# Kernel optimization log

Hardware: AMD Instinct MI355X
Metric: run time of the kernel (lower is better)

The kernel has to match this reference:

```python
import jax, jax.numpy as jnp
import numpy as np

WS = 7      # window size
SHIFT = 3   # shift size
H = 56
W = 56
NH = 16     # num heads


def _layernorm(x, g, b):
    m = x.mean(-1, keepdims=True)
    v = x.var(-1, keepdims=True)
    return (x - m) / jnp.sqrt(v + 1e-5) * g + b


def setup_inputs() -> dict:
    key = jax.random.key(0)
    ks = jax.random.split(key, 8)
    B, C = 16, 512
    DH = 4 * C
    s = 0.02
    x = jax.random.normal(ks[0], (B, H * W, C), jnp.float32)

    # relative position index (matches torch buffer construction)
    coords = np.stack(np.meshgrid(np.arange(WS), np.arange(WS), indexing='ij')).reshape(2, -1)
    rel = (coords[:, :, None] - coords[:, None, :]).transpose(1, 2, 0).copy()
    rel[..., 0] += WS - 1
    rel[..., 1] += WS - 1
    rel[..., 0] *= 2 * WS - 1
    rpi = jnp.asarray(rel.sum(-1), jnp.int32)  # (49, 49)

    # shifted-window additive attention mask (nW, N, N)
    img = np.zeros((H, W))
    cnt = 0
    for hs in (slice(0, -WS), slice(-WS, -SHIFT), slice(-SHIFT, None)):
        for wsl in (slice(0, -WS), slice(-WS, -SHIFT), slice(-SHIFT, None)):
            img[hs, wsl] = cnt
            cnt += 1
    mw = img.reshape(H // WS, WS, W // WS, WS).transpose(0, 2, 1, 3).reshape(-1, WS * WS)
    diff = mw[:, None, :] - mw[:, :, None]  # == mw.unsqueeze(1) - mw.unsqueeze(2)
    attn_mask = jnp.asarray(np.where(diff != 0, -100.0, 0.0), jnp.float32)

    return {
        'x': x,
        'rpi': rpi,
        'attn_mask': attn_mask,
        'norm1_g': jnp.ones((C,), jnp.float32),
        'norm1_b': jnp.zeros((C,), jnp.float32),
        'qkv_w': jax.random.normal(ks[1], (3 * C, C), jnp.float32) * s,
        'qkv_b': jnp.zeros((3 * C,), jnp.float32),
        'proj_w': jax.random.normal(ks[2], (C, C), jnp.float32) * s,
        'proj_b': jnp.zeros((C,), jnp.float32),
        'rpb_table': jax.random.normal(ks[3], ((2 * WS - 1) ** 2, NH), jnp.float32) * s,
        'norm2_g': jnp.ones((C,), jnp.float32),
        'norm2_b': jnp.zeros((C,), jnp.float32),
        'mlp_w1': jax.random.normal(ks[4], (DH, C), jnp.float32) * s,
        'mlp_b1': jnp.zeros((DH,), jnp.float32),
        'mlp_w2': jax.random.normal(ks[5], (C, DH), jnp.float32) * s,
        'mlp_b2': jnp.zeros((C,), jnp.float32),
    }


def reference(x, rpi, attn_mask, norm1_g, norm1_b, qkv_w, qkv_b, proj_w, proj_b,
              rpb_table, norm2_g, norm2_b, mlp_w1, mlp_b1, mlp_w2, mlp_b2):
    B, L, C = x.shape
    N = WS * WS
    nW = (H // WS) * (W // WS)
    hd = C // NH

    # --- attention branch ---
    h = _layernorm(x, norm1_g, norm1_b).reshape(B, H, W, C)
    h = jnp.roll(h, (-SHIFT, -SHIFT), axis=(1, 2))
    # window partition -> (B*nW, N, C)
    xw = h.reshape(B, H // WS, WS, W // WS, WS, C).transpose(0, 1, 3, 2, 4, 5).reshape(B * nW, N, C)

    qkv = (xw @ qkv_w.T + qkv_b).reshape(B * nW, N, 3, NH, hd).transpose(2, 0, 3, 1, 4)
    q, k, v = qkv[0], qkv[1], qkv[2]  # (B*nW, NH, N, hd)
    attn = jnp.einsum('bhnd,bhmd->bhnm', q * (hd ** -0.5), k)
    rpb = rpb_table[rpi].transpose(2, 0, 1)  # (NH, N, N)
    attn = attn + rpb[None]
    attn = attn.reshape(B, nW, NH, N, N) + attn_mask[None, :, None]
    attn = jax.nn.softmax(attn.reshape(B * nW, NH, N, N), axis=-1)
    o = jnp.einsum('bhnm,bhmd->bhnd', attn, v).transpose(0, 2, 1, 3).reshape(B * nW, N, C)
    o = o @ proj_w.T + proj_b
    # window reverse + unshift
    o = o.reshape(B, H // WS, W // WS, WS, WS, C).transpose(0, 1, 3, 2, 4, 5).reshape(B, H, W, C)
    o = jnp.roll(o, (SHIFT, SHIFT), axis=(1, 2)).reshape(B, L, C)

    x = x + o
    # --- MLP branch ---
    h2 = _layernorm(x, norm2_g, norm2_b)
    m = jax.nn.gelu(h2 @ mlp_w1.T + mlp_b1, approximate=False)
    return x + (m @ mlp_w2.T + mlp_b2)
```

## Files before the change

kernel.cpp:

```cpp
#include <hip/hip_runtime.h>
#include <hip/hip_bf16.h>

typedef __attribute__((ext_vector_type(8))) short bf16x8_t;
typedef __attribute__((ext_vector_type(4))) float f32x4_t;

__device__ __forceinline__ void gll16(const void* g, void* l) {
  __builtin_amdgcn_global_load_lds((const __attribute__((address_space(1))) void*)g,
                                   (__attribute__((address_space(3))) void*)l, 16, 0, 0);
}

__global__ __launch_bounds__(256) void k_cvt(const float* __restrict__ in,
                                             __hip_bfloat16* __restrict__ out, int n) {
  int i = blockIdx.x * 256 + threadIdx.x;
  if (i < n) out[i] = __float2bfloat16(in[i]);
}

__global__ __launch_bounds__(256) void k_cmb(const int* __restrict__ rpi,
                                             const float* __restrict__ tab,
                                             const float* __restrict__ mask,
                                             float* __restrict__ cmbp) {
  int idx = blockIdx.x * 256 + threadIdx.x;
  int jj = idx & 3, lane = (idx >> 2) & 63, tile = (idx >> 8) & 15;
  int h = (idx >> 12) & 15, w6 = idx >> 16;
  int r = (tile >> 2) * 16 + (lane >> 4) * 4 + jj;
  int c = (tile & 3) * 16 + (lane & 15);
  float v = -1e9f;
  if (r < 49 && c < 49) v = tab[rpi[r * 49 + c] * 16 + h] + mask[w6 * 2401 + r * 49 + c];
  cmbp[idx] = v;
}

template<int PERM>
__global__ __launch_bounds__(256) void k_ln(const float* __restrict__ in,
                                            const float* __restrict__ g,
                                            const float* __restrict__ bta,
                                            __hip_bfloat16* __restrict__ out) {
  int token = blockIdx.x;
  int t = threadIdx.x;
  const float2 v = ((const float2*)(in + (size_t)token * 512))[t];
  float s = v.x + v.y, sq = v.x * v.x + v.y * v.y;
  #pragma unroll
  for (int d = 1; d < 64; d <<= 1) { s += __shfl_xor(s, d); sq += __shfl_xor(sq, d); }
  __shared__ float ps[4], pq[4];
  int w = t >> 6;
  if ((t & 63) == 0) { ps[w] = s; pq[w] = sq; }
  __syncthreads();
  s  = ps[0] + ps[1] + ps[2] + ps[3];
  sq = pq[0] + pq[1] + pq[2] + pq[3];
  float mean = s * (1.f / 512.f);
  float inv = rsqrtf(sq * (1.f / 512.f) - mean * mean + 1e-5f);
  size_t dst;
  if (PERM) {
    int b = token / 3136, p = token - b * 3136;
    int i = p / 56, j = p - i * 56;
    int gi = (i + 53) % 56, gj = (j + 53) % 56;
    dst = ((size_t)(((b * 64) + (gi / 7) * 8 + (gj / 7)) * 49) + (gi % 7) * 7 + (gj % 7)) * 512;
  } else {
    dst = (size_t)token * 512;
  }
  int c = t * 2;
  out[dst + c]     = __float2bfloat16((v.x - mean) * inv * g[c] + bta[c]);
  out[dst + c + 1] = __float2bfloat16((v.y - mean) * inv * g[c + 1] + bta[c + 1]);
}

__global__ __launch_bounds__(256) void k_attn(const __hip_bfloat16* __restrict__ qkv,
                                              const float* __restrict__ cmbp,
                                              __hip_bfloat16* __restrict__ o) {
  __shared__ __align__(16) __hip_bfloat16 vt_all[4 * 32 * 72];
  __shared__ __align__(16) __hip_bfloat16 P_all[4 * 64 * 72];
  const int t = threadIdx.x, l = t & 63, w = t >> 6;
  const int bw = blockIdx.x;
  const int head = blockIdx.y * 4 + w;
  const int rr = l & 15, g = l >> 4;
  __hip_bfloat16* vt = vt_all + w * (32 * 72);
  __hip_bfloat16* P  = P_all  + w * (64 * 72);
  const __hip_bfloat16* base = qkv + (size_t)bw * 49 * 1536 + head * 32;
  const bf16x8_t zero8 = {};

  { int d = l >> 1, sg = (l & 1) * 8;
    *(bf16x8_t*)(vt + d * 72 + 48 + sg) = zero8; }
  __builtin_amdgcn_sched_barrier(0);
  #pragma unroll
  for (int it = 0; it < 4; ++it) {
    int idx = l + it * 64;
    if (idx < 196) {
      int j = idx >> 2, sg = (idx & 3) * 8;
      bf16x8_t vv = *(const bf16x8_t*)(base + 1024 + (size_t)j * 1536 + sg);
      #pragma unroll
      for (int s2 = 0; s2 < 8; ++s2) vt[(sg + s2) * 72 + j] = ((__hip_bfloat16*)&vv)[s2];
    }
  }
  bf16x8_t aq[4], bk[4];
  #pragma unroll
  for (int m = 0; m < 4; ++m) {
    int row = m * 16 + rr;
    aq[m] = (row < 49) ? *(const bf16x8_t*)(base + (size_t)row * 1536 + g * 8) : zero8;
    bk[m] = (row < 49) ? *(const bf16x8_t*)(base + 512 + (size_t)row * 1536 + g * 8) : zero8;
  }
  const float4* cp = (const float4*)(cmbp + (size_t)((bw & 63) * 16 + head) * 4096);
  f32x4_t S[4][4];
  #pragma unroll
  for (int tm = 0; tm < 4; ++tm)
    #pragma unroll
    for (int tn = 0; tn < 4; ++tn) {
      float4 cv = cp[(tm * 4 + tn) * 64 + l];
      f32x4_t c0 = { cv.x, cv.y, cv.z, cv.w };
      S[tm][tn] = __builtin_amdgcn_mfma_f32_16x16x32_bf16(aq[tm], bk[tn], c0, 0, 0, 0);
    }
  float sm[4][4];
  #pragma unroll
  for (int tm = 0; tm < 4; ++tm) {
    #pragma unroll
    for (int jj = 0; jj < 4; ++jj) {
      float v = fmaxf(fmaxf(S[tm][0][jj], S[tm][1][jj]), fmaxf(S[tm][2][jj], S[tm][3][jj]));
      v = fmaxf(v, __shfl_xor(v, 1));
      v = fmaxf(v, __shfl_xor(v, 2));
      v = fmaxf(v, __shfl_xor(v, 4));
      v = fmaxf(v, __shfl_xor(v, 8));
      float s = 0.f;
      #pragma unroll
      for (int tn = 0; tn < 4; ++tn) {
        float e = __expf(S[tm][tn][jj] - v);
        S[tm][tn][jj] = e;
        s += e;
      }
      s += __shfl_xor(s, 1); s += __shfl_xor(s, 2); s += __shfl_xor(s, 4); s += __shfl_xor(s, 8);
      sm[tm][jj] = s;
    }
  }
  #pragma unroll
  for (int tm = 0; tm < 4; ++tm)
    #pragma unroll
    for (int tn = 0; tn < 4; ++tn)
      #pragma unroll
      for (int jj = 0; jj < 4; ++jj)
        P[(tm * 16 + g * 4 + jj) * 72 + tn * 16 + rr] = __float2bfloat16(S[tm][tn][jj]);

  f32x4_t O[4][2] = {};
  #pragma unroll
  for (int ks = 0; ks < 2; ++ks) {
    bf16x8_t pa[4], vb[2];
    #pragma unroll
    for (int tm = 0; tm < 4; ++tm)
      pa[tm] = *(const bf16x8_t*)(P + (tm * 16 + rr) * 72 + ks * 32 + g * 8);
    #pragma unroll
    for (int tn = 0; tn < 2; ++tn)
      vb[tn] = *(const bf16x8_t*)(vt + (tn * 16 + rr) * 72 + ks * 32 + g * 8);
    #pragma unroll
    for (int tm = 0; tm < 4; ++tm)
      #pragma unroll
      for (int tn = 0; tn < 2; ++tn)
        O[tm][tn] = __builtin_amdgcn_mfma_f32_16x16x32_bf16(pa[tm], vb[tn], O[tm][tn], 0, 0, 0);
  }
  #pragma unroll
  for (int tm = 0; tm < 4; ++tm) {
    #pragma unroll
    for (int jj = 0; jj < 4; ++jj) {
      int r = tm * 16 + g * 4 + jj;
      if (r < 49) {
        float rcp = 1.f / sm[tm][jj];
        size_t ob = ((size_t)bw * 49 + r) * 512 + head * 32;
        o[ob + rr]      = __float2bfloat16(O[tm][0][jj] * rcp);
        o[ob + 16 + rr] = __float2bfloat16(O[tm][1][jj] * rcp);
      }
    }
  }
}

template<int EP>
__global__ __launch_bounds__(256) void gemm_bt(const __hip_bfloat16* __restrict__ A,
                                               const __hip_bfloat16* __restrict__ Bw,
                                               int K, int Ncols,
                                               const float* __restrict__ bias,
                                               __hip_bfloat16* __restrict__ obf,
                                               const float* __restrict__ resid,
                                               float* __restrict__ ofp) {
  __shared__ __align__(16) __hip_bfloat16 Ash[128 * 32];
  __shared__ __align__(16) __hip_bfloat16 Bsh[128 * 32];
  const int m0 = blockIdx.x * 128, n0 = blockIdx.y * 128;
  const int t = threadIdx.x, l = t & 63, w = t >> 6;
  const int wr = w >> 1, wc = w & 1;
  f32x4_t acc[4][4] = {};
  const __hip_bfloat16* Ab = A + (size_t)m0 * K;
  const __hip_bfloat16* Bb = Bw + (size_t)n0 * K;
  const int r0 = t >> 2, sg = (t & 3) * 8;
  const int kq = l >> 4, rr = l & 15;

  for (int k0 = 0; k0 < K; k0 += 32) {
    gll16(Ab + (size_t)r0 * K + k0 + sg, (char*)Ash + t * 16);
    gll16(Bb + (size_t)r0 * K + k0 + sg, (char*)Bsh + t * 16);
    gll16(Ab + (size_t)(r0 + 64) * K + k0 + sg, (char*)Ash + (t + 256) * 16);
    gll16(Bb + (size_t)(r0 + 64) * K + k0 + sg, (char*)Bsh + (t + 256) * 16);
    __syncthreads();
    const bf16x8_t* Af = (const bf16x8_t*)Ash;
    const bf16x8_t* Bf = (const bf16x8_t*)Bsh;
    bf16x8_t af[4], bfr[4];
    #pragma unroll
    for (int m = 0; m < 4; ++m) af[m] = Af[(wr * 64 + m * 16 + rr) * 4 + kq];
    #pragma unroll
    for (int n = 0; n < 4; ++n) bfr[n] = Bf[(wc * 64 + n * 16 + rr) * 4 + kq];
    #pragma unroll
    for (int m = 0; m < 4; ++m)
      #pragma unroll
      for (int n = 0; n < 4; ++n)
        acc[m][n] = __builtin_amdgcn_mfma_f32_16x16x32_bf16(af[m], bfr[n], acc[m][n], 0, 0, 0);
    __syncthreads();
  }

  #pragma unroll
  for (int m = 0; m < 4; ++m) {
    #pragma unroll
    for (int n = 0; n < 4; ++n) {
      const int gcol = n0 + wc * 64 + n * 16 + rr;
      #pragma unroll
      for (int j = 0; j < 4; ++j) {
        const int grow = m0 + wr * 64 + m * 16 + kq * 4 + j;
        float v = acc[m][n][j] + bias[gcol];
        if (EP == 0) {
          if (gcol < 512) v *= 0.17677669529663687f;
          obf[(size_t)grow * Ncols + gcol] = __float2bfloat16(v);
        } else if (EP == 1) {
          int bw = grow / 49, nn = grow - bw * 49;
          int b = bw >> 6, wi = bw & 63;
          int hh = (wi >> 3) * 7 + nn / 7 + 3;  if (hh >= 56) hh -= 56;
          int ww2 = (wi & 7) * 7 + (nn % 7) + 3; if (ww2 >= 56) ww2 -= 56;
          size_t tok = (size_t)b * 3136 + hh * 56 + ww2;
          ofp[tok * 512 + gcol] = resid[tok * 512 + gcol] + v;
        } else if (EP == 2) {
          float u = 0.5f * v * (1.f + erff(v * 0.70710678118f));
          obf[(size_t)grow * Ncols + gcol] = __float2bfloat16(u);
        } else {
          ofp[(size_t)grow * 512 + gcol] += v;
        }
      }
    }
  }
}

extern "C" void kernel_launch(void* const* d_in, const int* in_sizes, int n_in,
                              void* d_out, int out_size, void* d_ws, size_t ws_size,
                              hipStream_t stream) {
  const float* x      = (const float*)d_in[0];
  const int*   rpi    = (const int*)  d_in[1];
  const float* amask  = (const float*)d_in[2];
  const float* n1g    = (const float*)d_in[3];
  const float* n1b    = (const float*)d_in[4];
  const float* qkv_w  = (const float*)d_in[5];
  const float* qkv_b  = (const float*)d_in[6];
  const float* proj_w = (const float*)d_in[7];
  const float* proj_b = (const float*)d_in[8];
  const float* rpb_t  = (const float*)d_in[9];
  const float* n2g    = (const float*)d_in[10];
  const float* n2b    = (const float*)d_in[11];
  const float* w1     = (const float*)d_in[12];
  const float* b1     = (const float*)d_in[13];
  const float* w2     = (const float*)d_in[14];
  const float* b2     = (const float*)d_in[15];
  float* out = (float*)d_out;

  char* ws = (char*)d_ws;
  const size_t M = 50176;
  const size_t szA = M * 2048 * 2;
  const size_t szB = M * 1536 * 2;
  const size_t offB = szA;
  const size_t offW = offB + szB;
  __hip_bfloat16* bufA = (__hip_bfloat16*)(ws);
  __hip_bfloat16* bufB = (__hip_bfloat16*)(ws + offB);
  __hip_bfloat16* wqkv  = (__hip_bfloat16*)(ws + offW);
  __hip_bfloat16* wproj = wqkv + 786432;
  __hip_bfloat16* wm1   = wproj + 262144;
  __hip_bfloat16* wm2   = wm1 + 1048576;
  float* cmbp = (float*)(ws + szA - (size_t)4194304 * 4);

  k_cvt<<<3072, 256, 0, stream>>>(qkv_w, wqkv, 786432);
  k_cvt<<<1024, 256, 0, stream>>>(proj_w, wproj, 262144);
  k_cvt<<<4096, 256, 0, stream>>>(w1, wm1, 1048576);
  k_cvt<<<4096, 256, 0, stream>>>(w2, wm2, 1048576);
  k_cmb<<<16384, 256, 0, stream>>>(rpi, rpb_t, amask, cmbp);

  k_ln<1><<<50176, 256, 0, stream>>>(x, n1g, n1b, bufA);
  gemm_bt<0><<<dim3(392, 12), 256, 0, stream>>>(bufA, wqkv, 512, 1536, qkv_b, bufB, nullptr, nullptr);
  k_attn<<<dim3(1024, 4), 256, 0, stream>>>(bufB, cmbp, bufA);
  gemm_bt<1><<<dim3(392, 4), 256, 0, stream>>>(bufA, wproj, 512, 512, proj_b, nullptr, x, out);
  k_ln<0><<<50176, 256, 0, stream>>>(out, n2g, n2b, bufB);
  gemm_bt<2><<<dim3(392, 16), 256, 0, stream>>>(bufB, wm1, 512, 2048, b1, bufA, nullptr, nullptr);
  gemm_bt<3><<<dim3(392, 4), 256, 0, stream>>>(bufA, wm2, 2048, 512, b2, nullptr, nullptr, out);
}
```

Before: 893.2 us.

## Replace 128x128 GEMM with double-buffered 256x256 swizzled-LDS GEMM and XCD remap

Replaces the 128x128, single-buffered GEMM used for all four linear layers with a 256x256 tile, 512-thread kernel. It double-buffers LDS with a 64-wide K step and interleaves global-to-LDS staging of the next tile with MFMA work on the current one. It also XOR-swizzles the LDS layout to avoid bank conflicts, remaps workgroup IDs across the 8 XCDs for L2 locality, and raises wave priority around the MFMA blocks. The goal is more data reuse per load and latency hiding. The cost is 128KB of LDS per block, lower occupancy, and heavy register pressure.

```diff
diff --git a/kernel.cpp b/kernel.cpp
--- a/kernel.cpp
+++ b/kernel.cpp
@@ -167,73 +167,138 @@
 }
 
 template<int EP>
-__global__ __launch_bounds__(256) void gemm_bt(const __hip_bfloat16* __restrict__ A,
-                                               const __hip_bfloat16* __restrict__ Bw,
-                                               int K, int Ncols,
-                                               const float* __restrict__ bias,
-                                               __hip_bfloat16* __restrict__ obf,
-                                               const float* __restrict__ resid,
-                                               float* __restrict__ ofp) {
-  __shared__ __align__(16) __hip_bfloat16 Ash[128 * 32];
-  __shared__ __align__(16) __hip_bfloat16 Bsh[128 * 32];
-  const int m0 = blockIdx.x * 128, n0 = blockIdx.y * 128;
+__global__ __launch_bounds__(512, 2) void gemm256(const __hip_bfloat16* __restrict__ A,
+                                                  const __hip_bfloat16* __restrict__ Bw,
+                                                  int K, int Ncols, int nNB,
+                                                  const float* __restrict__ bias,
+                                                  __hip_bfloat16* __restrict__ obf,
+                                                  const float* __restrict__ resid,
+                                                  float* __restrict__ ofp) {
+  __shared__ __align__(16) char LDS[131072];
+  const int nwg = gridDim.x, orig = blockIdx.x;
+  const int q8 = nwg >> 3, r8 = nwg & 7;
+  const int xcd = orig & 7, lin = orig >> 3;
+  const int wgid = (xcd < r8 ? xcd * (q8 + 1) : r8 * (q8 + 1) + (xcd - r8) * q8) + lin;
+  const int bx = wgid / nNB, by = wgid - bx * nNB;
+  const int m0 = bx * 256, n0 = by * 256;
   const int t = threadIdx.x, l = t & 63, w = t >> 6;
-  const int wr = w >> 1, wc = w & 1;
-  f32x4_t acc[4][4] = {};
-  const __hip_bfloat16* Ab = A + (size_t)m0 * K;
-  const __hip_bfloat16* Bb = Bw + (size_t)n0 * K;
-  const int r0 = t >> 2, sg = (t & 3) * 8;
-  const int kq = l >> 4, rr = l & 15;
-
-  for (int k0 = 0; k0 < K; k0 += 32) {
-    gll16(Ab + (size_t)r0 * K + k0 + sg, (char*)Ash + t * 16);
-    gll16(Bb + (size_t)r0 * K + k0 + sg, (char*)Bsh + t * 16);
-    gll16(Ab + (size_t)(r0 + 64) * K + k0 + sg, (char*)Ash + (t + 256) * 16);
-    gll16(Bb + (size_t)(r0 + 64) * K + k0 + sg, (char*)Bsh + (t + 256) * 16);
+  const int wr = w >> 2, wc = w & 3;
+  const int rr = l & 15, kq = l >> 4;
+
+  int r0, c0, r1, c1;
+  { int d = t * 16; int sub = d >> 10, wr_ = (d & 1023) >> 6, wc_ = d & 63;
+    int cb = wc_ ^ ((wr_ & 8) << 2); r0 = (sub >> 1) * 16 + wr_; c0 = (sub & 1) * 32 + (cb >> 1); }
+  { int d = t * 16 + 8192; int sub = d >> 10, wr_ = (d & 1023) >> 6, wc_ = d & 63;
+    int cb = wc_ ^ ((wr_ & 8) << 2); r1 = (sub >> 1) * 16 + wr_; c1 = (sub & 1) * 32 + (cb >> 1); }
+  const size_t o0 = (size_t)r0 * K + c0, o1 = (size_t)r1 * K + c1;
+  const __hip_bfloat16* gA = A + (size_t)m0 * K;
+  const __hip_bfloat16* gB = Bw + (size_t)n0 * K;
+
+  auto stageA = [&](int buf, int h, int k0) {
+    char* dst = LDS + buf * 32768 + h * 16384;
+    const __hip_bfloat16* s = gA + (size_t)h * 128 * K + k0;
+    gll16(s + o0, dst + t * 16);
+    gll16(s + o1, dst + t * 16 + 8192);
+  };
+  auto stageB = [&](int buf, int h, int k0) {
+    char* dst = LDS + 65536 + buf * 32768 + h * 16384;
+    const __hip_bfloat16* s = gB + (size_t)h * 128 * K + k0;
+    gll16(s + o0, dst + t * 16);
+    gll16(s + o1, dst + t * 16 + 8192);
+  };
+
+  const char *baseA = nullptr, *baseB = nullptr;
+  auto ldA = [&](bf16x8_t (&ar)[4][2], int mq) {
+    #pragma unroll
+    for (int m = 0; m < 4; ++m)
+      #pragma unroll
+      for (int ks = 0; ks < 2; ++ks) {
+        int r = mq * 64 + m * 16 + rr;
+        int off = ((r >> 4) * 2 + ks) * 1024 + (r & 15) * 64 + ((kq * 16) ^ ((r & 8) << 2));
+        ar[m][ks] = *(const bf16x8_t*)(baseA + off);
+      }
+  };
+  auto ldB = [&](bf16x8_t (&br)[2][2], int nq) {
+    #pragma unroll
+    for (int n = 0; n < 2; ++n)
+      #pragma unroll
+      for (int ks = 0; ks < 2; ++ks) {
+        int r = (wc & 1) * 64 + nq * 32 + n * 16 + rr;
+        int off = ((r >> 4) * 2 + ks) * 1024 + (r & 15) * 64 + ((kq * 16) ^ ((r & 8) << 2));
+        br[n][ks] = *(const bf16x8_t*)(baseB + off);
+      }
+  };
+
+  f32x4_t a00[4][2] = {}, a01[4][2] = {}, a10[4][2] = {}, a11[4][2] = {};
+  auto mma = [&](f32x4_t (&ac)[4][2], bf16x8_t (&ar)[4][2], bf16x8_t (&br)[2][2]) {
+    __builtin_amdgcn_s_setprio(1);
+    #pragma unroll
+    for (int m = 0; m < 4; ++m)
+      #pragma unroll
+      for (int n = 0; n < 2; ++n)
+        #pragma unroll
+        for (int ks = 0; ks < 2; ++ks)
+          ac[m][n] = __builtin_amdgcn_mfma_f32_16x16x32_bf16(ar[m][ks], br[n][ks], ac[m][n], 0, 0, 0);
+    __builtin_amdgcn_s_setprio(0);
+  };
+
+  stageA(0, 0, 0); stageA(0, 1, 0); stageB(0, 0, 0); stageB(0, 1, 0);
+  __syncthreads();
+
+  const int NT = K >> 6;
+  int cur = 0;
+  for (int kt = 0; kt < NT; ++kt) {
+    const int nxt = cur ^ 1, k1 = (kt + 1) << 6;
+    const bool st = (kt + 1 < NT);
+    baseA = LDS + cur * 32768 + wr * 16384;
+    baseB = LDS + 65536 + cur * 32768 + (wc >> 1) * 16384;
+    bf16x8_t ar[4][2], br0[2][2], br1[2][2];
+    if (st) stageA(nxt, 0, k1);
+    ldA(ar, 0); ldB(br0, 0);
+    mma(a00, ar, br0);
+    if (st) stageA(nxt, 1, k1);
+    ldB(br1, 1);
+    mma(a01, ar, br1);
+    if (st) stageB(nxt, 0, k1);
+    ldA(ar, 1);
+    mma(a11, ar, br1);
+    if (st) stageB(nxt, 1, k1);
+    mma(a10, ar, br0);
     __syncthreads();
-    const bf16x8_t* Af = (const bf16x8_t*)Ash;
-    const bf16x8_t* Bf = (const bf16x8_t*)Bsh;
-    bf16x8_t af[4], bfr[4];
-    #pragma unroll
-    for (int m = 0; m < 4; ++m) af[m] = Af[(wr * 64 + m * 16 + rr) * 4 + kq];
-    #pragma unroll
-    for (int n = 0; n < 4; ++n) bfr[n] = Bf[(wc * 64 + n * 16 + rr) * 4 + kq];
-    #pragma unroll
-    for (int m = 0; m < 4; ++m)
-      #pragma unroll
-      for (int n = 0; n < 4; ++n)
-        acc[m][n] = __builtin_amdgcn_mfma_f32_16x16x32_bf16(af[m], bfr[n], acc[m][n], 0, 0, 0);
-    __syncthreads();
-  }
-
-  #pragma unroll
-  for (int m = 0; m < 4; ++m) {
-    #pragma unroll
-    for (int n = 0; n < 4; ++n) {
-      const int gcol = n0 + wc * 64 + n * 16 + rr;
-      #pragma unroll
-      for (int j = 0; j < 4; ++j) {
-        const int grow = m0 + wr * 64 + m * 16 + kq * 4 + j;
-        float v = acc[m][n][j] + bias[gcol];
-        if (EP == 0) {
-          if (gcol < 512) v *= 0.17677669529663687f;
-          obf[(size_t)grow * Ncols + gcol] = __float2bfloat16(v);
-        } else if (EP == 1) {
-          int bw = grow / 49, nn = grow - bw * 49;
-          int b = bw >> 6, wi = bw & 63;
-          int hh = (wi >> 3) * 7 + nn / 7 + 3;  if (hh >= 56) hh -= 56;
-          int ww2 = (wi & 7) * 7 + (nn % 7) + 3; if (ww2 >= 56) ww2 -= 56;
-          size_t tok = (size_t)b * 3136 + hh * 56 + ww2;
-          ofp[tok * 512 + gcol] = resid[tok * 512 + gcol] + v;
-        } else if (EP == 2) {
-          float u = 0.5f * v * (1.f + erff(v * 0.70710678118f));
-          obf[(size_t)grow * Ncols + gcol] = __float2bfloat16(u);
-        } else {
-          ofp[(size_t)grow * 512 + gcol] += v;
+    cur = nxt;
+  }
+
+  auto epi = [&](f32x4_t (&ac)[4][2], int mq, int nq) {
+    #pragma unroll
+    for (int m = 0; m < 4; ++m) {
+      #pragma unroll
+      for (int n = 0; n < 2; ++n) {
+        const int gcol = n0 + wc * 64 + nq * 32 + n * 16 + rr;
+        #pragma unroll
+        for (int j = 0; j < 4; ++j) {
+          const int grow = m0 + wr * 128 + mq * 64 + m * 16 + kq * 4 + j;
+          float v = ac[m][n][j] + bias[gcol];
+          if (EP == 0) {
+            if (gcol < 512) v *= 0.17677669529663687f;
+            obf[(size_t)grow * Ncols + gcol] = __float2bfloat16(v);
+          } else if (EP == 1) {
+            int bw = grow / 49, nn = grow - bw * 49;
+            int b = bw >> 6, wi = bw & 63;
+            int hh = (wi >> 3) * 7 + nn / 7 + 3;  if (hh >= 56) hh -= 56;
+            int ww2 = (wi & 7) * 7 + (nn % 7) + 3; if (ww2 >= 56) ww2 -= 56;
+            size_t tok = (size_t)b * 3136 + hh * 56 + ww2;
+            ofp[tok * 512 + gcol] = resid[tok * 512 + gcol] + v;
+          } else if (EP == 2) {
+            float u = 0.5f * v * (1.f + erff(v * 0.70710678118f));
+            obf[(size_t)grow * Ncols + gcol] = __float2bfloat16(u);
+          } else {
+            ofp[(size_t)grow * 512 + gcol] += v;
+          }
         }
       }
     }
-  }
+  };
+  epi(a00, 0, 0); epi(a01, 0, 1); epi(a10, 1, 0); epi(a11, 1, 1);
 }
 
 extern "C" void kernel_launch(void* const* d_in, const int* in_sizes, int n_in,
@@ -278,10 +343,10 @@
   k_cmb<<<16384, 256, 0, stream>>>(rpi, rpb_t, amask, cmbp);
 
   k_ln<1><<<50176, 256, 0, stream>>>(x, n1g, n1b, bufA);
-  gemm_bt<0><<<dim3(392, 12), 256, 0, stream>>>(bufA, wqkv, 512, 1536, qkv_b, bufB, nullptr, nullptr);
+  gemm256<0><<<196 * 6, 512, 0, stream>>>(bufA, wqkv, 512, 1536, 6, qkv_b, bufB, nullptr, nullptr);
   k_attn<<<dim3(1024, 4), 256, 0, stream>>>(bufB, cmbp, bufA);
-  gemm_bt<1><<<dim3(392, 4), 256, 0, stream>>>(bufA, wproj, 512, 512, proj_b, nullptr, x, out);
+  gemm256<1><<<196 * 2, 512, 0, stream>>>(bufA, wproj, 512, 512, 2, proj_b, nullptr, x, out);
   k_ln<0><<<50176, 256, 0, stream>>>(out, n2g, n2b, bufB);
-  gemm_bt<2><<<dim3(392, 16), 256, 0, stream>>>(bufB, wm1, 512, 2048, b1, bufA, nullptr, nullptr);
-  gemm_bt<3><<<dim3(392, 4), 256, 0, stream>>>(bufA, wm2, 2048, 512, b2, nullptr, nullptr, out);
-}
+  gemm256<2><<<196 * 8, 512, 0, stream>>>(bufB, wm1, 512, 2048, 8, b1, bufA, nullptr, nullptr);
+  gemm256<3><<<196 * 2, 512, 0, stream>>>(bufA, wm2, 2048, 512, 2, b2, nullptr, nullptr, out);
+}
```

Result: faster. 826.3 us (-7.5%).

## Replace GEMM with 256x256-tile, 4-stage pipelined, swizzled-LDS kernel with XCD remap

Applied to the files above, without the earlier changes.

Replaces the 128x128 single-buffered GEMM with a 256x256-tile kernel using 512 threads. K tiles are prefetched three deep into a 4-slot LDS ring via direct global-to-LDS loads, with explicit vmcnt waits and barriers. An XOR swizzle on LDS offsets avoids bank conflicts, s_setprio raises priority around the MFMA bursts, and a workgroup-id remap groups tiles per XCD to improve L2 locality. Each block holds more accumulators (8x4 per wave), which raises register pressure and uses 128KB of LDS, limiting occupancy, and the hand-placed waitcnts make correctness fragile.

```diff
diff --git a/kernel.cpp b/kernel.cpp
--- a/kernel.cpp
+++ b/kernel.cpp
@@ -167,53 +167,94 @@
 }
 
 template<int EP>
-__global__ __launch_bounds__(256) void gemm_bt(const __hip_bfloat16* __restrict__ A,
-                                               const __hip_bfloat16* __restrict__ Bw,
-                                               int K, int Ncols,
-                                               const float* __restrict__ bias,
-                                               __hip_bfloat16* __restrict__ obf,
-                                               const float* __restrict__ resid,
-                                               float* __restrict__ ofp) {
-  __shared__ __align__(16) __hip_bfloat16 Ash[128 * 32];
-  __shared__ __align__(16) __hip_bfloat16 Bsh[128 * 32];
-  const int m0 = blockIdx.x * 128, n0 = blockIdx.y * 128;
+__global__ __launch_bounds__(512, 2) void gemm256(const __hip_bfloat16* __restrict__ A,
+                                                  const __hip_bfloat16* __restrict__ Bw,
+                                                  int K, int Ncols, int nNB,
+                                                  const float* __restrict__ bias,
+                                                  __hip_bfloat16* __restrict__ obf,
+                                                  const float* __restrict__ resid,
+                                                  float* __restrict__ ofp) {
+  __shared__ __align__(16) char LDS[131072];
+  const int nwg = gridDim.x, orig = blockIdx.x;
+  const int q8 = nwg >> 3, r8 = nwg & 7;
+  const int xcd = orig & 7, lin = orig >> 3;
+  const int wgid = (xcd < r8 ? xcd * (q8 + 1) : r8 * (q8 + 1) + (xcd - r8) * q8) + lin;
+  const int bx = wgid / nNB, by = wgid - bx * nNB;
+  const int m0 = bx * 256, n0 = by * 256;
   const int t = threadIdx.x, l = t & 63, w = t >> 6;
-  const int wr = w >> 1, wc = w & 1;
-  f32x4_t acc[4][4] = {};
-  const __hip_bfloat16* Ab = A + (size_t)m0 * K;
-  const __hip_bfloat16* Bb = Bw + (size_t)n0 * K;
-  const int r0 = t >> 2, sg = (t & 3) * 8;
-  const int kq = l >> 4, rr = l & 15;
-
-  for (int k0 = 0; k0 < K; k0 += 32) {
-    gll16(Ab + (size_t)r0 * K + k0 + sg, (char*)Ash + t * 16);
-    gll16(Bb + (size_t)r0 * K + k0 + sg, (char*)Bsh + t * 16);
-    gll16(Ab + (size_t)(r0 + 64) * K + k0 + sg, (char*)Ash + (t + 256) * 16);
-    gll16(Bb + (size_t)(r0 + 64) * K + k0 + sg, (char*)Bsh + (t + 256) * 16);
-    __syncthreads();
-    const bf16x8_t* Af = (const bf16x8_t*)Ash;
-    const bf16x8_t* Bf = (const bf16x8_t*)Bsh;
-    bf16x8_t af[4], bfr[4];
-    #pragma unroll
-    for (int m = 0; m < 4; ++m) af[m] = Af[(wr * 64 + m * 16 + rr) * 4 + kq];
-    #pragma unroll
-    for (int n = 0; n < 4; ++n) bfr[n] = Bf[(wc * 64 + n * 16 + rr) * 4 + kq];
+  const int wr = w >> 2, wc = w & 3;
+  const int rr = l & 15, kq = l >> 4;
+  const int lofs = rr * 64 + ((kq * 16) ^ ((rr & 8) << 2));
+
+  size_t o0, o1;
+  { int d = t * 16; int r = (d >> 10) * 16 + ((d >> 6) & 15);
+    int cb = (d & 63) ^ (((d >> 9) & 1) << 5); o0 = (size_t)r * K + (cb >> 1); }
+  { int d = 8192 + t * 16; int r = (d >> 10) * 16 + ((d >> 6) & 15);
+    int cb = (d & 63) ^ (((d >> 9) & 1) << 5); o1 = (size_t)r * K + (cb >> 1); }
+  const __hip_bfloat16* gA = A + (size_t)m0 * K;
+  const __hip_bfloat16* gB = Bw + (size_t)n0 * K;
+
+  auto stage = [&](int tile, int half) {
+    int b = (tile & 3) * 16384 + half * 8192 + t * 16;
+    size_t o = (half ? o1 : o0) + (size_t)tile * 32;
+    gll16(gA + o, LDS + b);
+    gll16(gB + o, LDS + 65536 + b);
+  };
+
+  f32x4_t acc[8][4] = {};
+
+  stage(0, 0); stage(0, 1); stage(1, 0); stage(1, 1); stage(2, 0); stage(2, 1);
+  asm volatile("s_waitcnt vmcnt(8)" ::: "memory");
+  __builtin_amdgcn_s_barrier();
+
+  const int NT = K >> 5;
+  for (int kt = 0; kt < NT; ++kt) {
+    const char* bA = LDS + (kt & 3) * 16384 + wr * 8192;
+    const char* bB = LDS + 65536 + (kt & 3) * 16384 + wc * 4096;
+    bf16x8_t ar[4], br[4];
+    #pragma unroll
+    for (int m = 0; m < 4; ++m) ar[m] = *(const bf16x8_t*)(bA + m * 1024 + lofs);
+    #pragma unroll
+    for (int n = 0; n < 4; ++n) br[n] = *(const bf16x8_t*)(bB + n * 1024 + lofs);
+    if (kt + 3 < NT) stage(kt + 3, 0);
+    __builtin_amdgcn_s_barrier();
+    asm volatile("s_waitcnt lgkmcnt(0)" ::: "memory");
+    __builtin_amdgcn_sched_barrier(0);
+    __builtin_amdgcn_s_setprio(1);
     #pragma unroll
     for (int m = 0; m < 4; ++m)
       #pragma unroll
       for (int n = 0; n < 4; ++n)
-        acc[m][n] = __builtin_amdgcn_mfma_f32_16x16x32_bf16(af[m], bfr[n], acc[m][n], 0, 0, 0);
-    __syncthreads();
-  }
-
-  #pragma unroll
-  for (int m = 0; m < 4; ++m) {
+        acc[m][n] = __builtin_amdgcn_mfma_f32_16x16x32_bf16(ar[m], br[n], acc[m][n], 0, 0, 0);
+    __builtin_amdgcn_s_setprio(0);
+    __builtin_amdgcn_s_barrier();
+    #pragma unroll
+    for (int m = 0; m < 4; ++m) ar[m] = *(const bf16x8_t*)(bA + (4 + m) * 1024 + lofs);
+    if (kt + 3 < NT) stage(kt + 3, 1);
+    __builtin_amdgcn_s_barrier();
+    asm volatile("s_waitcnt lgkmcnt(0)" ::: "memory");
+    __builtin_amdgcn_sched_barrier(0);
+    __builtin_amdgcn_s_setprio(1);
+    #pragma unroll
+    for (int m = 0; m < 4; ++m)
+      #pragma unroll
+      for (int n = 0; n < 4; ++n)
+        acc[4 + m][n] = __builtin_amdgcn_mfma_f32_16x16x32_bf16(ar[m], br[n], acc[4 + m][n], 0, 0, 0);
+    __builtin_amdgcn_s_setprio(0);
+    if (kt + 3 < NT)      asm volatile("s_waitcnt vmcnt(8)" ::: "memory");
+    else if (kt + 2 < NT) asm volatile("s_waitcnt vmcnt(4)" ::: "memory");
+    else if (kt + 1 < NT) asm volatile("s_waitcnt vmcnt(0)" ::: "memory");
+    __builtin_amdgcn_s_barrier();
+  }
+
+  #pragma unroll
+  for (int m = 0; m < 8; ++m) {
     #pragma unroll
     for (int n = 0; n < 4; ++n) {
       const int gcol = n0 + wc * 64 + n * 16 + rr;
       #pragma unroll
       for (int j = 0; j < 4; ++j) {
-        const int grow = m0 + wr * 64 + m * 16 + kq * 4 + j;
+        const int grow = m0 + wr * 128 + m * 16 + kq * 4 + j;
         float v = acc[m][n][j] + bias[gcol];
         if (EP == 0) {
           if (gcol < 512) v *= 0.17677669529663687f;
@@ -278,10 +319,10 @@
   k_cmb<<<16384, 256, 0, stream>>>(rpi, rpb_t, amask, cmbp);
 
   k_ln<1><<<50176, 256, 0, stream>>>(x, n1g, n1b, bufA);
-  gemm_bt<0><<<dim3(392, 12), 256, 0, stream>>>(bufA, wqkv, 512, 1536, qkv_b, bufB, nullptr, nullptr);
+  gemm256<0><<<196 * 6, 512, 0, stream>>>(bufA, wqkv, 512, 1536, 6, qkv_b, bufB, nullptr, nullptr);
   k_attn<<<dim3(1024, 4), 256, 0, stream>>>(bufB, cmbp, bufA);
-  gemm_bt<1><<<dim3(392, 4), 256, 0, stream>>>(bufA, wproj, 512, 512, proj_b, nullptr, x, out);
+  gemm256<1><<<196 * 2, 512, 0, stream>>>(bufA, wproj, 512, 512, 2, proj_b, nullptr, x, out);
   k_ln<0><<<50176, 256, 0, stream>>>(out, n2g, n2b, bufB);
-  gemm_bt<2><<<dim3(392, 16), 256, 0, stream>>>(bufB, wm1, 512, 2048, b1, bufA, nullptr, nullptr);
-  gemm_bt<3><<<dim3(392, 4), 256, 0, stream>>>(bufA, wm2, 2048, 512, b2, nullptr, nullptr, out);
-}
+  gemm256<2><<<196 * 8, 512, 0, stream>>>(bufB, wm1, 512, 2048, 8, b1, bufA, nullptr, nullptr);
+  gemm256<3><<<196 * 2, 512, 0, stream>>>(bufA, wm2, 2048, 512, 2, b2, nullptr, nullptr, out);
+}
```

New measurement: 843.2 us. 1.06x faster.
